# Kernel optimization log

Hardware: AMD Instinct MI355X
Metric: run time of the kernel (lower is better)

Reference implementation:

```python
import jax, jax.numpy as jnp
import numpy as np

RATE = 0.1
INPUT_SHAPE = [8192]
BATCH_DIMS = 1
K = max(1, round(RATE * int(np.prod(INPUT_SHAPE))))  # 819


def setup_inputs() -> dict:
    key = jax.random.key(0)
    x = jax.random.normal(key, (4096, 8192), dtype=jnp.float32)
    return {"x": x}


def reference(x) -> jnp.ndarray:
    batch_flat = int(np.prod(x.shape[:BATCH_DIMS]))
    x_flat = x.reshape(batch_flat, -1)            # [B, D]
    ax = jnp.abs(x_flat)
    topk_vals, _ = jax.lax.top_k(ax, K)           # [B, K] sorted descending
    thr = topk_vals[:, -1:]                        # kth largest |x| per row
    mask = (ax >= thr).reshape(x.shape)
    return jnp.where(mask, x, jnp.zeros_like(x))
```

## Files before the change

kernel.cpp:

```cpp
#include <hip/hip_runtime.h>
#include <stdint.h>


constexpr int NCOLS = 8192;
constexpr int TPB   = 256;
constexpr int V4    = NCOLS / 4;
constexpr int VPT   = V4 / TPB;

constexpr int PAD = 8;
constexpr int B1 = 2048, C1 = 2;
constexpr int B2 = 1024, C2 = 4;
constexpr int S1 = B1 + PAD;
constexpr int S2 = B2 + PAD;
constexpr int HW = (C2 * S2 > C1 * S1) ? C2 * S2 : C1 * S1;

struct Shared {
  uint32_t hist[HW];
  uint32_t wavesum[4];
  uint32_t digit;
  uint32_t rem;
};

template <int BINS, int COPIES>
__device__ __forceinline__ uint32_t run_phase(Shared& sh, const uint4 (&v)[VPT],
                                              int dshift, int cshift, uint32_t cprefix,
                                              uint32_t& rem, int tid, int lane, int wave) {
  constexpr int BPT = BINS / TPB;
  constexpr int STRIDE = BINS + PAD;
  constexpr int ZW4 = (COPIES * STRIDE) / 4;

  uint4* hz = (uint4*)sh.hist;
  for (int i = tid; i < ZW4; i += TPB) hz[i] = make_uint4(0u, 0u, 0u, 0u);
  __syncthreads();

  uint32_t* h = &sh.hist[((wave * COPIES) >> 2) * STRIDE];
#pragma unroll
  for (int i = 0; i < VPT; ++i) {
    uint32_t a[4] = {v[i].x, v[i].y, v[i].z, v[i].w};
#pragma unroll
    for (int j = 0; j < 4; ++j) {
      uint32_t key = a[j] & 0x7fffffffu;
      if ((key >> cshift) == cprefix)
        atomicAdd(&h[(key >> dshift) & (BINS - 1)], 1u);
    }
  }
  __syncthreads();

  uint32_t hb[BPT];
#pragma unroll
  for (int j = 0; j < BPT; ++j) hb[j] = 0;
#pragma unroll
  for (int c = 0; c < COPIES; ++c) {
    const uint4* hp = (const uint4*)&sh.hist[c * STRIDE + tid * BPT];
#pragma unroll
    for (int q = 0; q < BPT / 4; ++q) {
      uint4 t = hp[q];
      hb[4 * q + 0] += t.x; hb[4 * q + 1] += t.y;
      hb[4 * q + 2] += t.z; hb[4 * q + 3] += t.w;
    }
  }
  uint32_t L = 0;
#pragma unroll
  for (int j = 0; j < BPT; ++j) L += hb[j];

  uint32_t suf = L;
#pragma unroll
  for (int off = 1; off < 64; off <<= 1) {
    uint32_t o = __shfl_down(suf, off, 64);
    suf += (lane + off < 64) ? o : 0u;
  }
  if (lane == 0) sh.wavesum[wave] = suf;
  __syncthreads();
  uint32_t addw = 0;
#pragma unroll
  for (int w = 0; w < 4; ++w) addw += (w > wave) ? sh.wavesum[w] : 0u;
  suf += addw;

  uint32_t s = suf - L;
#pragma unroll
  for (int j = BPT - 1; j >= 0; --j) {
    uint32_t snext = s;
    s += hb[j];
    if (s >= rem && snext < rem) {
      sh.digit = (uint32_t)(tid * BPT + j);
      sh.rem = rem - snext;
    }
  }
  __syncthreads();
  uint32_t d = sh.digit;
  rem = sh.rem;
  return d;
}

__global__ __launch_bounds__(TPB) void topk_row_kernel(const float* __restrict__ x,
                                                       float* __restrict__ out,
                                                       int K) {
  __shared__ Shared sh;
  const int row  = blockIdx.x;
  const int tid  = threadIdx.x;
  const int lane = tid & 63;
  const int wave = tid >> 6;

  const uint4* xr = (const uint4*)(x) + (size_t)row * V4;
  uint4 v[VPT];
#pragma unroll
  for (int i = 0; i < VPT; ++i) v[i] = xr[tid + i * TPB];

  uint32_t rem = (uint32_t)K;
  uint32_t d1 = run_phase<B1, C1>(sh, v, 20, 31, 0u, rem, tid, lane, wave);
  uint32_t d2 = run_phase<B2, C2>(sh, v, 10, 20, d1, rem, tid, lane, wave);
  uint32_t d3 = run_phase<B2, C2>(sh, v,  0, 10, (d1 << 10) | d2, rem, tid, lane, wave);

  const uint32_t thr = (d1 << 20) | (d2 << 10) | d3;

  uint4* outr = (uint4*)(out) + (size_t)row * V4;
#pragma unroll
  for (int i = 0; i < VPT; ++i) {
    uint4 o = v[i];
    o.x = ((o.x & 0x7fffffffu) >= thr) ? o.x : 0u;
    o.y = ((o.y & 0x7fffffffu) >= thr) ? o.y : 0u;
    o.z = ((o.z & 0x7fffffffu) >= thr) ? o.z : 0u;
    o.w = ((o.w & 0x7fffffffu) >= thr) ? o.w : 0u;
    outr[tid + i * TPB] = o;
  }
}

extern "C" void kernel_launch(void* const* d_in, const int* in_sizes, int n_in,
                              void* d_out, int out_size, void* d_ws, size_t ws_size,
                              hipStream_t stream) {
  (void)n_in; (void)out_size; (void)d_ws; (void)ws_size;
  const float* x = (const float*)d_in[0];
  float* out = (float*)d_out;
  const int rows = in_sizes[0] / NCOLS;
  const int K = (int)(0.1 * NCOLS + 0.5);
  topk_row_kernel<<<rows, TPB, 0, stream>>>(x, out, K);
}
```

Measured before the change: 231.5 us.

## Replace second and third radix passes with compacted candidate bitwise select

```diff
diff --git a/kernel.cpp b/kernel.cpp
--- a/kernel.cpp
+++ b/kernel.cpp
@@ -7,90 +7,21 @@
 constexpr int V4    = NCOLS / 4;
 constexpr int VPT   = V4 / TPB;
 
+constexpr int B1  = 2048;
+constexpr int C1  = 2;
 constexpr int PAD = 8;
-constexpr int B1 = 2048, C1 = 2;
-constexpr int B2 = 1024, C2 = 4;
-constexpr int S1 = B1 + PAD;
-constexpr int S2 = B2 + PAD;
-constexpr int HW = (C2 * S2 > C1 * S1) ? C2 * S2 : C1 * S1;
-
-struct Shared {
-  uint32_t hist[HW];
-  uint32_t wavesum[4];
+constexpr int S1  = B1 + PAD;
+constexpr int CAP = 512;
+
+typedef uint32_t u32x4 __attribute__((ext_vector_type(4)));
+
+struct alignas(16) Shared {
+  uint32_t hist[C1 * S1];
+  uint32_t wavered[4];
   uint32_t digit;
   uint32_t rem;
+  uint32_t thrlow;
 };
-
-template <int BINS, int COPIES>
-__device__ __forceinline__ uint32_t run_phase(Shared& sh, const uint4 (&v)[VPT],
-                                              int dshift, int cshift, uint32_t cprefix,
-                                              uint32_t& rem, int tid, int lane, int wave) {
-  constexpr int BPT = BINS / TPB;
-  constexpr int STRIDE = BINS + PAD;
-  constexpr int ZW4 = (COPIES * STRIDE) / 4;
-
-  uint4* hz = (uint4*)sh.hist;
-  for (int i = tid; i < ZW4; i += TPB) hz[i] = make_uint4(0u, 0u, 0u, 0u);
-  __syncthreads();
-
-  uint32_t* h = &sh.hist[((wave * COPIES) >> 2) * STRIDE];
-#pragma unroll
-  for (int i = 0; i < VPT; ++i) {
-    uint32_t a[4] = {v[i].x, v[i].y, v[i].z, v[i].w};
-#pragma unroll
-    for (int j = 0; j < 4; ++j) {
-      uint32_t key = a[j] & 0x7fffffffu;
-      if ((key >> cshift) == cprefix)
-        atomicAdd(&h[(key >> dshift) & (BINS - 1)], 1u);
-    }
-  }
-  __syncthreads();
-
-  uint32_t hb[BPT];
-#pragma unroll
-  for (int j = 0; j < BPT; ++j) hb[j] = 0;
-#pragma unroll
-  for (int c = 0; c < COPIES; ++c) {
-    const uint4* hp = (const uint4*)&sh.hist[c * STRIDE + tid * BPT];
-#pragma unroll
-    for (int q = 0; q < BPT / 4; ++q) {
-      uint4 t = hp[q];
-      hb[4 * q + 0] += t.x; hb[4 * q + 1] += t.y;
-      hb[4 * q + 2] += t.z; hb[4 * q + 3] += t.w;
-    }
-  }
-  uint32_t L = 0;
-#pragma unroll
-  for (int j = 0; j < BPT; ++j) L += hb[j];
-
-  uint32_t suf = L;
-#pragma unroll
-  for (int off = 1; off < 64; off <<= 1) {
-    uint32_t o = __shfl_down(suf, off, 64);
-    suf += (lane + off < 64) ? o : 0u;
-  }
-  if (lane == 0) sh.wavesum[wave] = suf;
-  __syncthreads();
-  uint32_t addw = 0;
-#pragma unroll
-  for (int w = 0; w < 4; ++w) addw += (w > wave) ? sh.wavesum[w] : 0u;
-  suf += addw;
-
-  uint32_t s = suf - L;
-#pragma unroll
-  for (int j = BPT - 1; j >= 0; --j) {
-    uint32_t snext = s;
-    s += hb[j];
-    if (s >= rem && snext < rem) {
-      sh.digit = (uint32_t)(tid * BPT + j);
-      sh.rem = rem - snext;
-    }
-  }
-  __syncthreads();
-  uint32_t d = sh.digit;
-  rem = sh.rem;
-  return d;
-}
 
 __global__ __launch_bounds__(TPB) void topk_row_kernel(const float* __restrict__ x,
                                                        float* __restrict__ out,
@@ -106,22 +37,166 @@
 #pragma unroll
   for (int i = 0; i < VPT; ++i) v[i] = xr[tid + i * TPB];
 
+  uint4* hz = (uint4*)sh.hist;
+  for (int i = tid; i < (C1 * S1) / 4; i += TPB) hz[i] = make_uint4(0u, 0u, 0u, 0u);
+  __syncthreads();
+
+  uint32_t* h = &sh.hist[(wave >> 1) * S1];
+#pragma unroll
+  for (int i = 0; i < VPT; ++i) {
+    atomicAdd(&h[(v[i].x & 0x7fffffffu) >> 20], 1u);
+    atomicAdd(&h[(v[i].y & 0x7fffffffu) >> 20], 1u);
+    atomicAdd(&h[(v[i].z & 0x7fffffffu) >> 20], 1u);
+    atomicAdd(&h[(v[i].w & 0x7fffffffu) >> 20], 1u);
+  }
+  __syncthreads();
+
+  uint32_t hb[8];
+  {
+    const uint4* p0 = (const uint4*)&sh.hist[0 * S1 + tid * 8];
+    const uint4* p1 = (const uint4*)&sh.hist[1 * S1 + tid * 8];
+    uint4 a0 = p0[0], a1 = p0[1], b0 = p1[0], b1 = p1[1];
+    hb[0] = a0.x + b0.x; hb[1] = a0.y + b0.y; hb[2] = a0.z + b0.z; hb[3] = a0.w + b0.w;
+    hb[4] = a1.x + b1.x; hb[5] = a1.y + b1.y; hb[6] = a1.z + b1.z; hb[7] = a1.w + b1.w;
+  }
+  uint32_t L = hb[0] + hb[1] + hb[2] + hb[3] + hb[4] + hb[5] + hb[6] + hb[7];
+
+  uint32_t suf = L;
+#pragma unroll
+  for (int off = 1; off < 64; off <<= 1) {
+    uint32_t o = __shfl_down(suf, off, 64);
+    suf += (lane + off < 64) ? o : 0u;
+  }
+  if (lane == 0) sh.wavered[wave] = suf;
+  __syncthreads();
+
   uint32_t rem = (uint32_t)K;
-  uint32_t d1 = run_phase<B1, C1>(sh, v, 20, 31, 0u, rem, tid, lane, wave);
-  uint32_t d2 = run_phase<B2, C2>(sh, v, 10, 20, d1, rem, tid, lane, wave);
-  uint32_t d3 = run_phase<B2, C2>(sh, v,  0, 10, (d1 << 10) | d2, rem, tid, lane, wave);
-
-  const uint32_t thr = (d1 << 20) | (d2 << 10) | d3;
-
-  uint4* outr = (uint4*)(out) + (size_t)row * V4;
+  {
+    uint32_t addw = 0;
+#pragma unroll
+    for (int w = 0; w < 4; ++w) addw += (w > wave) ? sh.wavered[w] : 0u;
+    suf += addw;
+    uint32_t s = suf - L;
+#pragma unroll
+    for (int j = 7; j >= 0; --j) {
+      uint32_t snx = s;
+      s += hb[j];
+      if (s >= rem && snx < rem) {
+        sh.digit = (uint32_t)(tid * 8 + j);
+        sh.rem   = rem - snx;
+      }
+    }
+  }
+  __syncthreads();
+  const uint32_t d1 = sh.digit;
+  rem = sh.rem;
+
+  uint32_t m = 0;
+#pragma unroll
+  for (int i = 0; i < VPT; ++i) {
+    m += ((v[i].x & 0x7fffffffu) >> 20) == d1;
+    m += ((v[i].y & 0x7fffffffu) >> 20) == d1;
+    m += ((v[i].z & 0x7fffffffu) >> 20) == d1;
+    m += ((v[i].w & 0x7fffffffu) >> 20) == d1;
+  }
+  uint32_t inc = m;
+#pragma unroll
+  for (int off = 1; off < 64; off <<= 1) {
+    uint32_t o = __shfl_up(inc, off, 64);
+    inc += (lane >= off) ? o : 0u;
+  }
+  uint32_t excl = inc - m;
+  if (lane == 63) sh.wavered[wave] = inc;
+  __syncthreads();
+
+  uint32_t n = 0, base = 0;
+#pragma unroll
+  for (int w = 0; w < 4; ++w) {
+    uint32_t t = sh.wavered[w];
+    n += t;
+    base += (w < wave) ? t : 0u;
+  }
+  {
+    uint32_t idx = base + excl;
+#pragma unroll
+    for (int i = 0; i < VPT; ++i) {
+      uint32_t a;
+      a = v[i].x & 0x7fffffffu; if ((a >> 20) == d1) { if (idx < CAP) sh.hist[idx] = a; ++idx; }
+      a = v[i].y & 0x7fffffffu; if ((a >> 20) == d1) { if (idx < CAP) sh.hist[idx] = a; ++idx; }
+      a = v[i].z & 0x7fffffffu; if ((a >> 20) == d1) { if (idx < CAP) sh.hist[idx] = a; ++idx; }
+      a = v[i].w & 0x7fffffffu; if ((a >> 20) == d1) { if (idx < CAP) sh.hist[idx] = a; ++idx; }
+    }
+  }
+  __syncthreads();
+
+  if (n <= CAP) {
+    if (wave == 0) {
+      uint32_t key[8];
+      uint32_t actm = 0;
+#pragma unroll
+      for (int j = 0; j < 8; ++j) {
+        int id = lane + 64 * j;
+        bool ok = id < (int)n;
+        key[j] = ok ? sh.hist[id] : 0u;
+        actm |= ok ? (1u << j) : 0u;
+      }
+      uint32_t p = 0, r = rem;
+      for (int b = 19; b >= 0; --b) {
+        uint32_t c1 = 0, tm = 0;
+#pragma unroll
+        for (int j = 0; j < 8; ++j) {
+          bool t = ((actm >> j) & 1u) && ((key[j] >> b) & 1u);
+          tm |= t ? (1u << j) : 0u;
+          c1 += (uint32_t)__popcll(__ballot(t));
+        }
+        if (c1 >= r) { p |= (1u << b); actm = tm; }
+        else         { r -= c1; actm &= ~tm; }
+      }
+      if (lane == 0) sh.thrlow = p;
+    }
+    __syncthreads();
+  } else {
+    uint32_t p = 0, r = rem;
+    for (int b = 19; b >= 0; --b) {
+      const uint32_t msk  = 0x7fffffffu & ~((1u << (b + 1)) - 1u);
+      const uint32_t want = ((d1 << 20) | p) & msk;
+      uint32_t c = 0;
+#pragma unroll
+      for (int i = 0; i < VPT; ++i) {
+        c += (((v[i].x & 0x7fffffffu) & msk) == want) && ((v[i].x >> b) & 1u);
+        c += (((v[i].y & 0x7fffffffu) & msk) == want) && ((v[i].y >> b) & 1u);
+        c += (((v[i].z & 0x7fffffffu) & msk) == want) && ((v[i].z >> b) & 1u);
+        c += (((v[i].w & 0x7fffffffu) & msk) == want) && ((v[i].w >> b) & 1u);
+      }
+      uint32_t t = c;
+#pragma unroll
+      for (int off = 1; off < 64; off <<= 1) {
+        uint32_t o = __shfl_down(t, off, 64);
+        t += (lane + off < 64) ? o : 0u;
+      }
+      if (lane == 0) sh.wavered[wave] = t;
+      __syncthreads();
+      uint32_t c1 = sh.wavered[0] + sh.wavered[1] + sh.wavered[2] + sh.wavered[3];
+      if (c1 >= r) p |= (1u << b);
+      else         r -= c1;
+      __syncthreads();
+    }
+    if (tid == 0) sh.thrlow = p;
+    __syncthreads();
+  }
+
+  const uint32_t thr = (d1 << 20) | sh.thrlow;
+
+  u32x4* outr = (u32x4*)(out) + (size_t)row * V4;
 #pragma unroll
   for (int i = 0; i < VPT; ++i) {
     uint4 o = v[i];
-    o.x = ((o.x & 0x7fffffffu) >= thr) ? o.x : 0u;
-    o.y = ((o.y & 0x7fffffffu) >= thr) ? o.y : 0u;
-    o.z = ((o.z & 0x7fffffffu) >= thr) ? o.z : 0u;
-    o.w = ((o.w & 0x7fffffffu) >= thr) ? o.w : 0u;
-    outr[tid + i * TPB] = o;
+    u32x4 w;
+    w.x = ((o.x & 0x7fffffffu) >= thr) ? o.x : 0u;
+    w.y = ((o.y & 0x7fffffffu) >= thr) ? o.y : 0u;
+    w.z = ((o.z & 0x7fffffffu) >= thr) ? o.z : 0u;
+    w.w = ((o.w & 0x7fffffffu) >= thr) ? o.w : 0u;
+    __builtin_nontemporal_store(w, &outr[tid + i * TPB]);
   }
 }
 
```

Result: no change. 235.6 us (+1.8%).
